# Kernel tuning notes

Hardware: AMD Instinct MI355X
Metric: run time of the kernel (lower is better)

The kernel has to match this reference:

```python
import jax, jax.numpy as jnp
import numpy as np

LEAKY_SLOPE = 0.01

def bilinear_interpolate(grid, coords):
    # grid: [H, W, C]; coords: [N, 2] in [0,1] (x, y order as in torch code)
    H = grid.shape[0] - 1
    W = grid.shape[1] - 1
    fx = coords[:, 0] * W
    fy = coords[:, 1] * H
    x0 = fx.astype(jnp.int32)
    y0 = fy.astype(jnp.int32)
    xf = jnp.mod(fx, 1.0)
    yf = jnp.mod(fy, 1.0)
    x1 = jnp.minimum(x0 + 1, W)
    y1 = jnp.minimum(y0 + 1, H)
    tl = grid[y0, x0]  # [N, C]
    tr = grid[y0, x1]
    bl = grid[y1, x0]
    br = grid[y1, x1]
    xf = xf[:, None]
    yf = yf[:, None]
    top = (1.0 - xf) * tl + xf * tr
    bot = (1.0 - xf) * bl + xf * br
    return (1.0 - yf) * top + yf * bot


def setup_inputs() -> dict:
    key = jax.random.key(0)
    ks = jax.random.split(key, 10)
    N = 2097152
    pos = jax.random.uniform(ks[0], (N, 2), dtype=jnp.float32)
    dir = jax.random.uniform(ks[1], (N, 2), dtype=jnp.float32)
    pos_grid = jax.random.normal(ks[2], (256, 256, 3), dtype=jnp.float32) * 10.0
    dir_grid = jax.random.normal(ks[3], (256, 256, 3), dtype=jnp.float32) * 10.0
    # Linear layers: PyTorch default init U(-1/sqrt(fan_in), 1/sqrt(fan_in))
    def linear(kw, kb, fan_in, fan_out):
        bound = 1.0 / np.sqrt(fan_in)
        W = jax.random.uniform(kw, (fan_out, fan_in), minval=-bound, maxval=bound, dtype=jnp.float32)
        b = jax.random.uniform(kb, (fan_out,), minval=-bound, maxval=bound, dtype=jnp.float32)
        return W, b
    W1, b1 = linear(ks[4], ks[5], 6, 64)
    W2, b2 = linear(ks[6], ks[7], 64, 64)
    W3, b3 = linear(ks[8], ks[9], 64, 1)
    return {"pos": pos, "dir": dir, "pos_grid": pos_grid, "dir_grid": dir_grid,
            "W1": W1, "b1": b1, "W2": W2, "b2": b2, "W3": W3, "b3": b3}


def reference(pos, dir, pos_grid, dir_grid, W1, b1, W2, b2, W3, b3):
    pos_feat = jax.lax.stop_gradient(bilinear_interpolate(pos_grid, pos))  # .detach() in torch
    dir_feat = jax.lax.stop_gradient(bilinear_interpolate(dir_grid, dir))
    x = jnp.concatenate([pos_feat, dir_feat], axis=1)  # [N, 6]
    x = jax.nn.leaky_relu(x @ W1.T + b1, LEAKY_SLOPE)
    x = jax.nn.leaky_relu(x @ W2.T + b2, LEAKY_SLOPE)
    return jax.nn.sigmoid(x @ W3.T + b3)  # [N, 1]
```

## Files before the change

### kernel.cpp

```cpp
#include <hip/hip_runtime.h>
#include <hip/hip_bf16.h>
#include <math.h>


#define NTHREADS 256
#define NB 4

typedef __attribute__((ext_vector_type(4))) short s16x4;
typedef __attribute__((ext_vector_type(8))) short s16x8;
typedef __attribute__((ext_vector_type(8))) __bf16 bf16x8;
typedef __attribute__((ext_vector_type(4))) float f32x4;
typedef __attribute__((ext_vector_type(2))) float f32x2;
typedef __attribute__((ext_vector_type(4))) int i32x4;
typedef __attribute__((ext_vector_type(2))) int i32x2;

static __device__ __forceinline__ short f2bf(float f) {
    return __builtin_bit_cast(short, __float2bfloat16(f));
}
static __device__ __forceinline__ int pk2(float lo, float hi) {
    unsigned short l = (unsigned short)f2bf(lo);
    unsigned short h = (unsigned short)f2bf(hi);
    return (int)(((unsigned int)h << 16) | (unsigned int)l);
}
static __device__ __forceinline__ int cvt_pk_bf16(float a, float b) {
    int r;
    asm("v_cvt_pk_bf16_f32 %0, %1, %2" : "=v"(r) : "v"(a), "v"(b));
    return r;
}
static __device__ __forceinline__ f32x2 pk_fma(f32x2 a, f32x2 b, f32x2 c) {
    f32x2 d;
    asm("v_pk_fma_f32 %0, %1, %2, %3" : "=v"(d) : "v"(a), "v"(b), "v"(c));
    return d;
}
static __device__ __forceinline__ f32x2 pk_mul(f32x2 a, f32x2 b) {
    f32x2 d;
    asm("v_pk_mul_f32 %0, %1, %2" : "=v"(d) : "v"(a), "v"(b));
    return d;
}
static __device__ __forceinline__ float fractf_hw(float x) {
    float r;
    asm("v_fract_f32 %0, %1" : "=v"(r) : "v"(x));
    return r;
}
static __device__ __forceinline__ float bflo(int u) {
    return __builtin_bit_cast(float, u << 16);
}
static __device__ __forceinline__ float bfhi(int u) {
    return __builtin_bit_cast(float, (int)(u & 0xffff0000));
}
static __device__ __forceinline__ int opaq(int x) {
    asm volatile("" : "+v"(x));
    return x;
}

__global__ __launch_bounds__(256) void make_patches(
    const float* __restrict__ gP, const float* __restrict__ gD,
    int* __restrict__ outP, int* __restrict__ outD) {
    int gid = blockIdx.x * 256 + threadIdx.x;
    const float* g = (gid < 65536) ? gP : gD;
    int* po = (gid < 65536) ? outP : outD;
    int id = gid & 65535;
    int y0 = id >> 8, x0 = id & 255;
    int x1 = min(x0 + 1, 255), y1 = min(y0 + 1, 255);
    const float* tl = g + (y0 * 256 + x0) * 3;
    const float* tr = g + (y0 * 256 + x1) * 3;
    const float* bl = g + (y1 * 256 + x0) * 3;
    const float* br = g + (y1 * 256 + x1) * 3;
    i32x4 u0;
    i32x2 u1;
    u0[0] = pk2(tl[0], bl[0]);
    u0[1] = pk2(tl[1], bl[1]);
    u0[2] = pk2(tl[2], bl[2]);
    u0[3] = pk2(tr[0], br[0]);
    u1[0] = pk2(tr[1], br[1]);
    u1[1] = pk2(tr[2], br[2]);
    *(i32x4*)(po + id * 8) = u0;
    *(i32x2*)(po + id * 8 + 4) = u1;
}

__global__ void pack_weights(const float* __restrict__ W1,
                             const float* __restrict__ b1,
                             const float* __restrict__ W2,
                             int* __restrict__ wt1, int* __restrict__ wt2) {
    int lane = threadIdx.x;
    int c = lane & 15, q = lane >> 4, q4 = q * 4;
#pragma unroll
    for (int mt = 0; mt < 4; ++mt) {
        int f = mt * 16 + c;
        float v[4];
#pragma unroll
        for (int j = 0; j < 4; ++j) {
            int k = q4 + j;
            float x = 0.0f;
            if (k < 6) x = W1[f * 6 + k];
            else if (k == 6) x = b1[f];
            v[j] = x;
        }
        wt1[lane * 8 + mt * 2 + 0] = pk2(v[0], v[1]);
        wt1[lane * 8 + mt * 2 + 1] = pk2(v[2], v[3]);
    }
#pragma unroll
    for (int kt2 = 0; kt2 < 2; ++kt2)
#pragma unroll
        for (int mt = 0; mt < 4; ++mt) {
            int n2 = mt * 16 + c;
            float v[8];
#pragma unroll
            for (int j2 = 0; j2 < 8; ++j2) {
                int k = kt2 * 32 + ((j2 >> 2) * 16) + q4 + (j2 & 3);
                v[j2] = W2[n2 * 64 + k];
            }
            int base = lane * 32 + (kt2 * 4 + mt) * 4;
#pragma unroll
            for (int h = 0; h < 4; ++h)
                wt2[base + h] = pk2(v[2 * h], v[2 * h + 1]);
        }
}

static __device__ __forceinline__ void patch_issue(
    const int* __restrict__ tab, float px, float py, int* P, float& xf,
    float& yf) {
    float fx = px * 255.0f;
    float fy = py * 255.0f;
    int x0 = (int)fx;
    int y0 = (int)fy;
    xf = fractf_hw(fx);
    yf = fractf_hw(fy);
    int idx = (y0 << 8) | x0;
    i32x4 a = *(const i32x4*)(tab + idx * 8);
    i32x2 b = *(const i32x2*)(tab + idx * 8 + 4);
    P[0] = a[0]; P[1] = a[1]; P[2] = a[2];
    P[3] = a[3]; P[4] = b[0]; P[5] = b[1];
}

static __device__ __forceinline__ void patch_lerp(const int* P, float xf,
                                                  float yf, float* f) {
#pragma unroll
    for (int ch = 0; ch < 3; ++ch) {
        float tl = bflo(P[ch]), bl = bfhi(P[ch]);
        float tr = bflo(P[ch + 3]), br = bfhi(P[ch + 3]);
        float top = fmaf(xf, tr - tl, tl);
        float bot = fmaf(xf, br - bl, bl);
        f[ch] = fmaf(yf, bot - top, top);
    }
}

__global__ __launch_bounds__(NTHREADS, 4) void mlp_mfma_kernel(
    const float* __restrict__ pos, const float* __restrict__ dir,
    const int* __restrict__ patP, const int* __restrict__ patD,
    const int* __restrict__ wt1, const int* __restrict__ wt2,
    const float* __restrict__ b2, const float* __restrict__ W3,
    const float* __restrict__ b3, float* __restrict__ out) {
    __shared__ int lds_F[4 * 64 * 4];
    __shared__ __align__(16) float cw[64];

    const int tid = threadIdx.x;
    if (tid < 64) cw[tid] = W3[tid];
    __syncthreads();

    const int w = tid >> 6;
    const int lane = tid & 63;
    const int c = lane & 15;
    const int q = lane >> 4;
    const int q4 = q * 4;

    int* FB = lds_F + w * (64 * 4);

    s16x4 A1f[4];
#pragma unroll
    for (int mt = 0; mt < 4; ++mt)
        A1f[mt] = __builtin_bit_cast(
            s16x4, *(const i32x2*)(wt1 + lane * 8 + mt * 2));
    s16x8 A2f[2][4];
#pragma unroll
    for (int kt2 = 0; kt2 < 2; ++kt2)
#pragma unroll
        for (int mt = 0; mt < 4; ++mt)
            A2f[kt2][mt] = __builtin_bit_cast(
                s16x8,
                *(const i32x4*)(wt2 + lane * 32 + (kt2 * 4 + mt) * 4));
    f32x4 ci[4];
#pragma unroll
    for (int mt = 0; mt < 4; ++mt)
        ci[mt] = *(const f32x4*)(b2 + mt * 16 + q4);

    const float b3s = b3[0];
    const int dbias = pk2(1.0f, 0.0f);
    const f32x2 c001 = {0.01f, 0.01f};

    const long wave_global = (long)blockIdx.x * 4 + w;
    const long base0 = wave_global * (64L * NB);
    const float2* pos2 = (const float2*)pos;
    const float2* dir2 = (const float2*)dir;

    float2 cp = pos2[base0 + lane];
    float2 cd = dir2[base0 + lane];

#pragma unroll 1
    for (int ib = 0; ib < NB; ++ib) {
        const long base = base0 + ib * 64;

        int P0_[12];
        float fr0[4];
        patch_issue(patP, cp.x, cp.y, P0_, fr0[0], fr0[1]);
        patch_issue(patD, cd.x, cd.y, P0_ + 6, fr0[2], fr0[3]);

        {
            int mb = min(ib + 1, NB - 1);
            cp = pos2[base0 + mb * 64 + lane];
            cd = dir2[base0 + mb * 64 + lane];
        }

        {
            float feat[6];
            patch_lerp(P0_, fr0[0], fr0[1], feat);
            patch_lerp(P0_ + 6, fr0[2], fr0[3], feat + 3);
            i32x4 dv;
            dv[0] = cvt_pk_bf16(feat[0], feat[1]);
            dv[1] = cvt_pk_bf16(feat[2], feat[3]);
            dv[2] = cvt_pk_bf16(feat[4], feat[5]);
            dv[3] = dbias;
            *(i32x4*)(FB + lane * 4) = dv;
        }

        float s[4];
#pragma unroll
        for (int t = 0; t < 4; ++t) {
            i32x2 bi = *(const i32x2*)(FB + (t * 16 + c) * 4 + (q & 1) * 2);
            s16x4 bfeat = __builtin_bit_cast(s16x4, bi);

            const f32x4 zacc = {0.f, 0.f, 0.f, 0.f};
            f32x4 a1[4];
#pragma unroll
            for (int mt = 0; mt < 4; ++mt)
                a1[mt] = __builtin_amdgcn_mfma_f32_16x16x16bf16_1k(
                    A1f[mt], bfeat, zacc, 0, 0, 0);

            i32x4 bbi[2];
#pragma unroll
            for (int kt2 = 0; kt2 < 2; ++kt2)
#pragma unroll
                for (int h = 0; h < 2; ++h) {
                    f32x4 x = a1[kt2 * 2 + h];
                    f32x2 xlo = {x[0], x[1]}, xhi = {x[2], x[3]};
                    f32x2 ylo = pk_mul(xlo, c001);
                    f32x2 yhi = pk_mul(xhi, c001);
                    float l0 = fmaxf(x[0], ylo[0]);
                    float l1 = fmaxf(x[1], ylo[1]);
                    float l2 = fmaxf(x[2], yhi[0]);
                    float l3 = fmaxf(x[3], yhi[1]);
                    bbi[kt2][h * 2 + 0] = cvt_pk_bf16(l0, l1);
                    bbi[kt2][h * 2 + 1] = cvt_pk_bf16(l2, l3);
                }

            f32x4 a2[4];
#pragma unroll
            for (int mt = 0; mt < 4; ++mt) a2[mt] = ci[mt];
#pragma unroll
            for (int kt2 = 0; kt2 < 2; ++kt2) {
                bf16x8 bb = __builtin_bit_cast(bf16x8, bbi[kt2]);
#pragma unroll
                for (int mt = 0; mt < 4; ++mt)
                    a2[mt] = __builtin_amdgcn_mfma_f32_16x16x32_bf16(
                        __builtin_bit_cast(bf16x8, A2f[kt2][mt]), bb, a2[mt],
                        0, 0, 0);
            }

            f32x2 tx = {0.f, 0.f}, ta = {0.f, 0.f};
            const float* cww = cw + opaq(q4);
#pragma unroll
            for (int mt = 0; mt < 4; ++mt) {
                const f32x4 wv = *(const f32x4*)(cww + mt * 16);
                f32x2 w0 = {wv[0], wv[1]}, w1 = {wv[2], wv[3]};
                f32x4 x = a2[mt];
                i32x4 xb = __builtin_bit_cast(i32x4, x);
                i32x4 ab = {xb[0] & 0x7fffffff, xb[1] & 0x7fffffff,
                            xb[2] & 0x7fffffff, xb[3] & 0x7fffffff};
                f32x4 xa = __builtin_bit_cast(f32x4, ab);
                f32x2 xlo = {x[0], x[1]}, xhi = {x[2], x[3]};
                f32x2 alo = {xa[0], xa[1]}, ahi = {xa[2], xa[3]};
                tx = pk_fma(xlo, w0, tx);
                tx = pk_fma(xhi, w1, tx);
                ta = pk_fma(alo, w0, ta);
                ta = pk_fma(ahi, w1, ta);
            }
            float tt = fmaf(0.505f, tx[0] + tx[1],
                            0.495f * (ta[0] + ta[1]));
            tt += __shfl_xor(tt, 16, 64);
            tt += __shfl_xor(tt, 32, 64);
            s[t] = tt;
        }

        float sa = (q & 1) ? s[1] : s[0];
        float sb = (q & 1) ? s[3] : s[2];
        float v = (q & 2) ? sb : sa;
        v += b3s;
        v = 1.0f / (1.0f + __expf(-v));
        out[base + q * 16 + c] = v;
    }
}

extern "C" void kernel_launch(void* const* d_in, const int* in_sizes, int n_in,
                              void* d_out, int out_size, void* d_ws,
                              size_t ws_size, hipStream_t stream) {
    const float* pos = (const float*)d_in[0];
    const float* dir = (const float*)d_in[1];
    const float* pos_grid = (const float*)d_in[2];
    const float* dir_grid = (const float*)d_in[3];
    const float* W1 = (const float*)d_in[4];
    const float* b1 = (const float*)d_in[5];
    const float* W2 = (const float*)d_in[6];
    const float* b2 = (const float*)d_in[7];
    const float* W3 = (const float*)d_in[8];
    const float* b3 = (const float*)d_in[9];
    float* out = (float*)d_out;

    int* patP = (int*)d_ws;
    int* patD = patP + 65536 * 8;
    int* wt1 = patD + 65536 * 8;
    int* wt2 = wt1 + 512;

    make_patches<<<512, 256, 0, stream>>>(pos_grid, dir_grid, patP, patD);
    pack_weights<<<1, 64, 0, stream>>>(W1, b1, W2, wt1, wt2);

    const int n = in_sizes[0] / 2;
    const int batches = n / 64;
    const int waves = batches / NB;
    const int blocks = waves / 4;

    mlp_mfma_kernel<<<blocks, NTHREADS, 0, stream>>>(
        pos, dir, patP, patD, wt1, wt2, b2, W3, b3, out);
}
```

Measured before the change: 142.4 us.

## Move layer-2 weights and bias to LDS, raise occupancy, merge prep kernels

Layer-2 MFMA weight fragments and the b2 bias are no longer held in registers for the whole kernel. They are staged once per block in padded LDS and reloaded every tile, which frees VGPRs so the launch-bounds target can rise from 4 to 5 blocks per CU. The weight packing kernel is also folded into the patch-building kernel to save one launch. The trade-off is extra LDS reads per tile and more LDS per block, which could offset the occupancy gain.

Result: slower. 164.7 us (+15.7%).

```diff
diff --git a/kernel.cpp b/kernel.cpp
--- a/kernel.cpp
+++ b/kernel.cpp
@@ -55,66 +55,65 @@
 
 __global__ __launch_bounds__(256) void make_patches(
     const float* __restrict__ gP, const float* __restrict__ gD,
-    int* __restrict__ outP, int* __restrict__ outD) {
+    const float* __restrict__ W1, const float* __restrict__ b1,
+    const float* __restrict__ W2, int* __restrict__ outP,
+    int* __restrict__ outD, int* __restrict__ wt1, int* __restrict__ wt2) {
     int gid = blockIdx.x * 256 + threadIdx.x;
-    const float* g = (gid < 65536) ? gP : gD;
-    int* po = (gid < 65536) ? outP : outD;
-    int id = gid & 65535;
-    int y0 = id >> 8, x0 = id & 255;
-    int x1 = min(x0 + 1, 255), y1 = min(y0 + 1, 255);
-    const float* tl = g + (y0 * 256 + x0) * 3;
-    const float* tr = g + (y0 * 256 + x1) * 3;
-    const float* bl = g + (y1 * 256 + x0) * 3;
-    const float* br = g + (y1 * 256 + x1) * 3;
-    i32x4 u0;
-    i32x2 u1;
-    u0[0] = pk2(tl[0], bl[0]);
-    u0[1] = pk2(tl[1], bl[1]);
-    u0[2] = pk2(tl[2], bl[2]);
-    u0[3] = pk2(tr[0], br[0]);
-    u1[0] = pk2(tr[1], br[1]);
-    u1[1] = pk2(tr[2], br[2]);
-    *(i32x4*)(po + id * 8) = u0;
-    *(i32x2*)(po + id * 8 + 4) = u1;
-}
-
-__global__ void pack_weights(const float* __restrict__ W1,
-                             const float* __restrict__ b1,
-                             const float* __restrict__ W2,
-                             int* __restrict__ wt1, int* __restrict__ wt2) {
-    int lane = threadIdx.x;
-    int c = lane & 15, q = lane >> 4, q4 = q * 4;
-#pragma unroll
-    for (int mt = 0; mt < 4; ++mt) {
-        int f = mt * 16 + c;
-        float v[4];
-#pragma unroll
-        for (int j = 0; j < 4; ++j) {
-            int k = q4 + j;
-            float x = 0.0f;
-            if (k < 6) x = W1[f * 6 + k];
-            else if (k == 6) x = b1[f];
-            v[j] = x;
+    if (gid < 131072) {
+        const float* g = (gid < 65536) ? gP : gD;
+        int* po = (gid < 65536) ? outP : outD;
+        int id = gid & 65535;
+        int y0 = id >> 8, x0 = id & 255;
+        int x1 = min(x0 + 1, 255), y1 = min(y0 + 1, 255);
+        const float* tl = g + (y0 * 256 + x0) * 3;
+        const float* tr = g + (y0 * 256 + x1) * 3;
+        const float* bl = g + (y1 * 256 + x0) * 3;
+        const float* br = g + (y1 * 256 + x1) * 3;
+        i32x4 u0;
+        i32x2 u1;
+        u0[0] = pk2(tl[0], bl[0]);
+        u0[1] = pk2(tl[1], bl[1]);
+        u0[2] = pk2(tl[2], bl[2]);
+        u0[3] = pk2(tr[0], br[0]);
+        u1[0] = pk2(tr[1], br[1]);
+        u1[1] = pk2(tr[2], br[2]);
+        *(i32x4*)(po + id * 8) = u0;
+        *(i32x2*)(po + id * 8 + 4) = u1;
+    } else if (gid < 131136) {
+        int lane = gid - 131072;
+        int c = lane & 15, q = lane >> 4, q4 = q * 4;
+#pragma unroll
+        for (int mt = 0; mt < 4; ++mt) {
+            int f = mt * 16 + c;
+            float v[4];
+#pragma unroll
+            for (int j = 0; j < 4; ++j) {
+                int k = q4 + j;
+                float x = 0.0f;
+                if (k < 6) x = W1[f * 6 + k];
+                else if (k == 6) x = b1[f];
+                v[j] = x;
+            }
+            wt1[lane * 8 + mt * 2 + 0] = pk2(v[0], v[1]);
+            wt1[lane * 8 + mt * 2 + 1] = pk2(v[2], v[3]);
         }
-        wt1[lane * 8 + mt * 2 + 0] = pk2(v[0], v[1]);
-        wt1[lane * 8 + mt * 2 + 1] = pk2(v[2], v[3]);
+#pragma unroll
+        for (int kt2 = 0; kt2 < 2; ++kt2)
+#pragma unroll
+            for (int mt = 0; mt < 4; ++mt) {
+                int n2 = mt * 16 + c;
+                float v[8];
+#pragma unroll
+                for (int j2 = 0; j2 < 8; ++j2) {
+                    int k = kt2 * 32 + ((j2 >> 2) * 16) + q4 + (j2 & 3);
+                    v[j2] = W2[n2 * 64 + k];
+                }
+                int base = lane * 32 + (kt2 * 4 + mt) * 4;
+#pragma unroll
+                for (int h = 0; h < 4; ++h)
+                    wt2[base + h] = pk2(v[2 * h], v[2 * h + 1]);
+            }
     }
-#pragma unroll
-    for (int kt2 = 0; kt2 < 2; ++kt2)
-#pragma unroll
-        for (int mt = 0; mt < 4; ++mt) {
-            int n2 = mt * 16 + c;
-            float v[8];
-#pragma unroll
-            for (int j2 = 0; j2 < 8; ++j2) {
-                int k = kt2 * 32 + ((j2 >> 2) * 16) + q4 + (j2 & 3);
-                v[j2] = W2[n2 * 64 + k];
-            }
-            int base = lane * 32 + (kt2 * 4 + mt) * 4;
-#pragma unroll
-            for (int h = 0; h < 4; ++h)
-                wt2[base + h] = pk2(v[2 * h], v[2 * h + 1]);
-        }
 }
 
 static __device__ __forceinline__ void patch_issue(
@@ -145,17 +144,23 @@
     }
 }
 
-__global__ __launch_bounds__(NTHREADS, 4) void mlp_mfma_kernel(
+__global__ __launch_bounds__(NTHREADS, 5) void mlp_mfma_kernel(
     const float* __restrict__ pos, const float* __restrict__ dir,
     const int* __restrict__ patP, const int* __restrict__ patD,
     const int* __restrict__ wt1, const int* __restrict__ wt2,
     const float* __restrict__ b2, const float* __restrict__ W3,
     const float* __restrict__ b3, float* __restrict__ out) {
     __shared__ int lds_F[4 * 64 * 4];
-    __shared__ __align__(16) float cw[64];
+    __shared__ __align__(16) float cw[128];
+    __shared__ __align__(16) int wt2_lds[64 * 36];
 
     const int tid = threadIdx.x;
-    if (tid < 64) cw[tid] = W3[tid];
+    if (tid < 128) cw[tid] = (tid < 64) ? b2[tid] : W3[tid - 64];
+#pragma unroll
+    for (int g = tid; g < 2048; g += 256) {
+        int ls = g >> 5, off = g & 31;
+        wt2_lds[ls * 36 + off] = wt2[g];
+    }
     __syncthreads();
 
     const int w = tid >> 6;
@@ -165,24 +170,13 @@
     const int q4 = q * 4;
 
     int* FB = lds_F + w * (64 * 4);
+    const int wb = lane * 36;
 
     s16x4 A1f[4];
 #pragma unroll
     for (int mt = 0; mt < 4; ++mt)
         A1f[mt] = __builtin_bit_cast(
             s16x4, *(const i32x2*)(wt1 + lane * 8 + mt * 2));
-    s16x8 A2f[2][4];
-#pragma unroll
-    for (int kt2 = 0; kt2 < 2; ++kt2)
-#pragma unroll
-        for (int mt = 0; mt < 4; ++mt)
-            A2f[kt2][mt] = __builtin_bit_cast(
-                s16x8,
-                *(const i32x4*)(wt2 + lane * 32 + (kt2 * 4 + mt) * 4));
-    f32x4 ci[4];
-#pragma unroll
-    for (int mt = 0; mt < 4; ++mt)
-        ci[mt] = *(const f32x4*)(b2 + mt * 16 + q4);
 
     const float b3s = b3[0];
     const int dbias = pk2(1.0f, 0.0f);
@@ -228,6 +222,14 @@
         for (int t = 0; t < 4; ++t) {
             i32x2 bi = *(const i32x2*)(FB + (t * 16 + c) * 4 + (q & 1) * 2);
             s16x4 bfeat = __builtin_bit_cast(s16x4, bi);
+
+            i32x4 A2r[8];
+            {
+                const int wbo = opaq(wb);
+#pragma unroll
+                for (int i = 0; i < 8; ++i)
+                    A2r[i] = *(const i32x4*)(wt2_lds + wbo + i * 4);
+            }
 
             const f32x4 zacc = {0.f, 0.f, 0.f, 0.f};
             f32x4 a1[4];
@@ -254,20 +256,24 @@
                 }
 
             f32x4 a2[4];
-#pragma unroll
-            for (int mt = 0; mt < 4; ++mt) a2[mt] = ci[mt];
+            {
+                const float* cwb = cw + opaq(q4);
+#pragma unroll
+                for (int mt = 0; mt < 4; ++mt)
+                    a2[mt] = *(const f32x4*)(cwb + mt * 16);
+            }
 #pragma unroll
             for (int kt2 = 0; kt2 < 2; ++kt2) {
                 bf16x8 bb = __builtin_bit_cast(bf16x8, bbi[kt2]);
 #pragma unroll
                 for (int mt = 0; mt < 4; ++mt)
                     a2[mt] = __builtin_amdgcn_mfma_f32_16x16x32_bf16(
-                        __builtin_bit_cast(bf16x8, A2f[kt2][mt]), bb, a2[mt],
-                        0, 0, 0);
+                        __builtin_bit_cast(bf16x8, A2r[kt2 * 4 + mt]), bb,
+                        a2[mt], 0, 0, 0);
             }
 
             f32x2 tx = {0.f, 0.f}, ta = {0.f, 0.f};
-            const float* cww = cw + opaq(q4);
+            const float* cww = cw + opaq(64 + q4);
 #pragma unroll
             for (int mt = 0; mt < 4; ++mt) {
                 const f32x4 wv = *(const f32x4*)(cww + mt * 16);
@@ -320,8 +326,8 @@
     int* wt1 = patD + 65536 * 8;
     int* wt2 = wt1 + 512;
 
-    make_patches<<<512, 256, 0, stream>>>(pos_grid, dir_grid, patP, patD);
-    pack_weights<<<1, 64, 0, stream>>>(W1, b1, W2, wt1, wt2);
+    make_patches<<<513, 256, 0, stream>>>(pos_grid, dir_grid, W1, b1, W2,
+                                          patP, patD, wt1, wt2);
 
     const int n = in_sizes[0] / 2;
     const int batches = n / 64;
```
